# Kernel tuning notes

Measured on AMD Instinct MI355X. Metric: run time of the kernel, lower is better.

The kernel has to match this reference:

```python
import jax, jax.numpy as jnp
import numpy as np

DIM = 2048
N_HEADS = 16
HEAD_DIM = 128
EPS = 1e-6


def setup_inputs() -> dict:
    key = jax.random.key(0)
    ks = jax.random.split(key, 8)
    b, gf, gh, gw = 1, 8, 16, 24
    s = gf * gh * gw
    c = HEAD_DIM // 2
    w = lambda k: 0.02 * jax.random.normal(k, (DIM, DIM), jnp.float32)
    return {
        "x": jax.random.normal(ks[0], (b, s, DIM), jnp.float32),
        "freqs_angle": jax.random.normal(ks[1], (1024, c), jnp.float32),
        "Wq": w(ks[2]), "bq": jnp.zeros((DIM,), jnp.float32),
        "Wk": w(ks[3]), "bk": jnp.zeros((DIM,), jnp.float32),
        "Wv": w(ks[4]), "bv": jnp.zeros((DIM,), jnp.float32),
        "Wo": w(ks[5]), "bo": jnp.zeros((DIM,), jnp.float32),
        "gq": jnp.ones((DIM,), jnp.float32),
        "gk": jnp.ones((DIM,), jnp.float32),
        "seq_len": s, "grid_f": gf, "grid_h": gh, "grid_w": gw,
    }


def _rms(t, g):
    return t * jax.lax.rsqrt(jnp.mean(t * t, axis=-1, keepdims=True) + EPS) * g


def _grid_angles(freqs_angle, gf, gh, gw, c):
    # band split [c - 2*(c//3), c//3, c//3] as in rope_apply
    cf = c - 2 * (c // 3)
    ch = cw = c // 3
    af = freqs_angle[:gf, :cf]            # [F, cf]
    ah = freqs_angle[:gh, cf:cf + ch]     # [H, ch]
    aw = freqs_angle[:gw, cf + ch:c]      # [W, cw]
    ang = jnp.concatenate([
        jnp.broadcast_to(af[:, None, None, :], (gf, gh, gw, cf)),
        jnp.broadcast_to(ah[None, :, None, :], (gf, gh, gw, ch)),
        jnp.broadcast_to(aw[None, None, :, :], (gf, gh, gw, cw)),
    ], axis=-1)
    return ang.reshape(gf * gh * gw, c)   # [s, c]


def reference(x, freqs_angle, Wq, bq, Wk, bk, Wv, bv, Wo, bo, gq, gk,
              seq_len, grid_f, grid_h, grid_w):
    b, s, _ = x.shape
    n, d = N_HEADS, HEAD_DIM
    c = d // 2
    ang = _grid_angles(freqs_angle, grid_f, grid_h, grid_w, c)
    cos = jnp.cos(ang)[None, :, None, :]  # [1, s, 1, c]
    sin = jnp.sin(ang)[None, :, None, :]

    def rope(t):  # complex multiply on (even, odd) = (real, imag) pairs
        te, to = t[..., 0::2], t[..., 1::2]
        return jnp.stack([te * cos - to * sin, te * sin + to * cos], axis=-1).reshape(t.shape)

    q = _rms(x @ Wq.T + bq, gq).reshape(b, s, n, d)
    k = _rms(x @ Wk.T + bk, gk).reshape(b, s, n, d)
    v = (x @ Wv.T + bv).reshape(b, s, n, d)
    q, k = rope(q), rope(k)

    scale = np.float32(1.0 / np.sqrt(d))
    scores = jnp.einsum('bqnd,bknd->bnqk', q, k) * scale
    p = jax.nn.softmax(scores, axis=-1)
    o = jnp.einsum('bnqk,bknd->bqnd', p, v).reshape(b, s, n * d)
    return o @ Wo.T + bo
```

## Files before the change

### kernel.cpp

```cpp
#include <hip/hip_runtime.h>
#include <stdint.h>
#include <stddef.h>

typedef __bf16 bf16_t;
typedef __bf16 bf16x8 __attribute__((ext_vector_type(8)));
typedef __bf16 bf16x4 __attribute__((ext_vector_type(4)));
typedef __bf16 bf16x2 __attribute__((ext_vector_type(2)));
typedef float  f32x4  __attribute__((ext_vector_type(4)));
typedef float  f32x16 __attribute__((ext_vector_type(16)));

#define SEQ   3072
#define DIMD  2048
#define NH    16
#define HD    128
#define QKVN  6144

__device__ __forceinline__ void async16(const bf16_t* g, bf16_t* l) {
  __builtin_amdgcn_global_load_lds((const __attribute__((address_space(1))) uint32_t*)g,
                                   (__attribute__((address_space(3))) uint32_t*)l, 16, 0, 0);
}

__global__ __launch_bounds__(256) void cvt_all(const float* __restrict__ x,
                                               const float* __restrict__ Wq,
                                               const float* __restrict__ Wk,
                                               const float* __restrict__ Wv,
                                               const float* __restrict__ Wo,
                                               const float* __restrict__ bq,
                                               const float* __restrict__ bk,
                                               const float* __restrict__ bv,
                                               bf16_t* __restrict__ xb,
                                               bf16_t* __restrict__ Wqkvb,
                                               bf16_t* __restrict__ Wob,
                                               float* __restrict__ bqkv) {
  const int b = blockIdx.x;
  const float* src; bf16_t* dst; int off;
  if (b < 3072)       { src = x;  dst = xb;              off = b; }
  else if (b < 5120)  { src = Wq; dst = Wqkvb;           off = b - 3072; }
  else if (b < 7168)  { src = Wk; dst = Wqkvb + 4194304; off = b - 5120; }
  else if (b < 9216)  { src = Wv; dst = Wqkvb + 8388608; off = b - 7168; }
  else if (b < 11264) { src = Wo; dst = Wob;             off = b - 9216; }
  else {
    int t = (b - 11264) * 256 + threadIdx.x;
    float v;
    if (t < 2048)      v = bq[t];
    else if (t < 4096) v = bk[t - 2048];
    else               v = bv[t - 4096];
    bqkv[t] = v;
    return;
  }
  const int idx = (off * 256 + threadIdx.x) * 8;
  const float4 a = *(const float4*)(src + idx);
  const float4 c = *(const float4*)(src + idx + 4);
  bf16x8 o;
  o[0] = (bf16_t)a.x; o[1] = (bf16_t)a.y; o[2] = (bf16_t)a.z; o[3] = (bf16_t)a.w;
  o[4] = (bf16_t)c.x; o[5] = (bf16_t)c.y; o[6] = (bf16_t)c.z; o[7] = (bf16_t)c.w;
  *(bf16x8*)(dst + idx) = o;
}

template<bool OUT_BF16>
__global__ __launch_bounds__(256, 3) void gemm_nt(const bf16_t* __restrict__ A,
                                                  const bf16_t* __restrict__ B,
                                                  const float* __restrict__ bias,
                                                  void* __restrict__ Cout,
                                                  int M, int N, int K) {
  __shared__ __align__(16) bf16_t As[128 * 64];
  __shared__ __align__(16) bf16_t Bs[128 * 64];
  const int t = threadIdx.x;
  const int lane = t & 63, wave = t >> 6;
  const int quad = lane >> 4, l15 = lane & 15;
  const int wy = wave >> 1, wx = wave & 1;
  const size_t bm = (size_t)blockIdx.y * 128, bn = (size_t)blockIdx.x * 128;
  const bf16_t* Ab = A + bm * K;
  const bf16_t* Bb = B + bn * K;
  f32x4 acc[4][4] = {};
  int srow[4], scol[4];
#pragma unroll
  for (int r = 0; r < 4; r++) {
    int L = r * 256 + t;
    int row = L >> 3, cp = L & 7;
    srow[r] = row;
    scol[r] = (cp ^ (row & 7)) * 8;
  }
  for (int k0 = 0; k0 < K; k0 += 64) {
    __syncthreads();
#pragma unroll
    for (int r = 0; r < 4; r++)
      async16(Ab + (size_t)srow[r] * K + k0 + scol[r], &As[(r * 256 + t) * 8]);
#pragma unroll
    for (int r = 0; r < 4; r++)
      async16(Bb + (size_t)srow[r] * K + k0 + scol[r], &Bs[(r * 256 + t) * 8]);
    __syncthreads();
#pragma unroll
    for (int ks = 0; ks < 2; ks++) {
      bf16x8 af[4], bfv[4];
#pragma unroll
      for (int i = 0; i < 4; i++) {
        int row = wy * 64 + i * 16 + l15;
        af[i] = *(const bf16x8*)&As[row * 64 + (((ks * 4 + quad) ^ (row & 7)) * 8)];
      }
#pragma unroll
      for (int j = 0; j < 4; j++) {
        int row = wx * 64 + j * 16 + l15;
        bfv[j] = *(const bf16x8*)&Bs[row * 64 + (((ks * 4 + quad) ^ (row & 7)) * 8)];
      }
#pragma unroll
      for (int i = 0; i < 4; i++)
#pragma unroll
        for (int j = 0; j < 4; j++)
          acc[i][j] = __builtin_amdgcn_mfma_f32_16x16x32_bf16(af[i], bfv[j], acc[i][j], 0, 0, 0);
    }
  }
#pragma unroll
  for (int i = 0; i < 4; i++) {
#pragma unroll
    for (int j = 0; j < 4; j++) {
      size_t row = bm + wy * 64 + i * 16 + quad * 4;
      size_t col = bn + wx * 64 + j * 16 + l15;
      float bb = bias[col];
#pragma unroll
      for (int r = 0; r < 4; r++) {
        float v = acc[i][j][r] + bb;
        if (OUT_BF16) ((bf16_t*)Cout)[(row + r) * N + col] = (bf16_t)v;
        else          ((float*)Cout)[(row + r) * N + col] = v;
      }
    }
  }
}

__global__ __launch_bounds__(256) void rmsrope(bf16_t* __restrict__ qkv,
                                               bf16_t* __restrict__ pk,
                                               const float* __restrict__ gq,
                                               const float* __restrict__ gk,
                                               const float* __restrict__ freqs) {
  const int s = blockIdx.x, t = threadIdx.x;
  bf16_t* row = qkv + (size_t)s * QKVN;
  bf16x8 qv = *(const bf16x8*)&row[t * 8];
  bf16x8 kv = *(const bf16x8*)&row[2048 + t * 8];
  float qf[8], kf[8];
  float qs = 0.f, ks2 = 0.f;
#pragma unroll
  for (int i = 0; i < 8; i++) {
    qf[i] = (float)qv[i]; qs  += qf[i] * qf[i];
    kf[i] = (float)kv[i]; ks2 += kf[i] * kf[i];
  }
#pragma unroll
  for (int m = 1; m < 64; m <<= 1) {
    qs  += __shfl_xor(qs, m);
    ks2 += __shfl_xor(ks2, m);
  }
  __shared__ float red[2][4];
  const int wave = t >> 6, lane = t & 63;
  if (lane == 0) { red[0][wave] = qs; red[1][wave] = ks2; }
  __syncthreads();
  qs  = red[0][0] + red[0][1] + red[0][2] + red[0][3];
  ks2 = red[1][0] + red[1][1] + red[1][2] + red[1][3];
  const float qsc = rsqrtf(qs  / 2048.f + 1e-6f) * 0.12751745f;
  const float ksc = rsqrtf(ks2 / 2048.f + 1e-6f);
  const int sf = s / 384, rem = s - sf * 384;
  const int sh = rem / 24, sw = rem - sh * 24;
  bf16x8 qo, ko;
#pragma unroll
  for (int u = 0; u < 4; u++) {
    const int col = t * 8 + 2 * u;
    const int i = (col >> 1) & 63;
    const int frow = (i < 22) ? sf : ((i < 43) ? sh : sw);
    const float ang = freqs[frow * 64 + i];
    float sn, cs;
    __sincosf(ang, &sn, &cs);
    float te = qf[2 * u]     * qsc * gq[col];
    float to = qf[2 * u + 1] * qsc * gq[col + 1];
    qo[2 * u]     = (bf16_t)(te * cs - to * sn);
    qo[2 * u + 1] = (bf16_t)(te * sn + to * cs);
    te = kf[2 * u]     * ksc * gk[col];
    to = kf[2 * u + 1] * ksc * gk[col + 1];
    ko[2 * u]     = (bf16_t)(te * cs - to * sn);
    ko[2 * u + 1] = (bf16_t)(te * sn + to * cs);
  }
  *(bf16x8*)&row[t * 8] = qo;
  *(bf16x8*)&pk[((size_t)(t >> 4) * SEQ + s) * HD + (t & 15) * 8] = ko;
}

__global__ __launch_bounds__(256) void vtrans(const bf16_t* __restrict__ qkv,
                                              bf16_t* __restrict__ pvt) {
  __shared__ bf16_t tile[128][65];
  const int h = blockIdx.y;
  const int s0 = blockIdx.x * 64;
  const int t = threadIdx.x;
#pragma unroll
  for (int r = 0; r < 4; r++) {
    int L = r * 256 + t, s = L >> 4, cp = L & 15;
    bf16x8 v = *(const bf16x8*)&qkv[(size_t)(s0 + s) * QKVN + 4096 + h * HD + cp * 8];
#pragma unroll
    for (int i = 0; i < 8; i++) tile[cp * 8 + i][s] = v[i];
  }
  __syncthreads();
#pragma unroll
  for (int r = 0; r < 4; r++) {
    int L = r * 256 + t, d = L >> 3, c = L & 7;
    bf16x8 o;
#pragma unroll
    for (int i = 0; i < 8; i++) o[i] = tile[d][c * 8 + i];
    *(bf16x8*)&pvt[((size_t)h * HD + d) * SEQ + s0 + c * 8] = o;
  }
}

#define STAGE_KV(BUF, KV1) do {                                              \
    _Pragma("unroll")                                                        \
    for (int r = 0; r < 5; r++) {                                            \
      int L = r * 192 + t;                                                   \
      async16(pkh + (size_t)(KV1) * HD + koff[r], &Ks[BUF][L * 8]);          \
      async16(pvh + (KV1) + voff[r], &Vt[BUF][L * 8]);                       \
    }                                                                        \
    if (t < 64) {                                                            \
      int L = 5 * 192 + t;                                                   \
      async16(pkh + (size_t)(KV1) * HD + koff[5], &Ks[BUF][L * 8]);          \
      async16(pvh + (KV1) + voff[5], &Vt[BUF][L * 8]);                       \
    }                                                                        \
  } while (0)

__global__ __launch_bounds__(192, 2) void flash_attn(const bf16_t* __restrict__ qkv,
                                                     const bf16_t* __restrict__ pk,
                                                     const bf16_t* __restrict__ pvt,
                                                     bf16_t* __restrict__ ob) {
  __shared__ __align__(16) bf16_t Ks[2][64 * 128];
  __shared__ __align__(16) bf16_t Vt[2][128 * 64];
  const int hh = blockIdx.y, qt = blockIdx.x;
  const int s0 = qt * 96;
  const int t = threadIdx.x, wave = t >> 6, lane = t & 63;
  const int l31 = lane & 31, hl = lane >> 5;
  const int wq = wave * 32;
  const bf16_t* pkh = pk  + (size_t)hh * (SEQ * HD);
  const bf16_t* pvh = pvt + (size_t)hh * (HD * SEQ);
  int koff[6], voff[6];
#pragma unroll
  for (int r = 0; r < 6; r++) {
    int L = r * 192 + t;
    int krow = L >> 4, kc = (L & 15) ^ (krow & 7);
    koff[r] = krow * HD + kc * 8;
    int vd = L >> 3, vc = (L & 7) ^ (vd & 7);
    voff[r] = vd * SEQ + vc * 8;
  }
  bf16x8 qfr[8];
#pragma unroll
  for (int ks = 0; ks < 8; ks++)
    qfr[ks] = *(const bf16x8*)&qkv[(size_t)(s0 + wq + l31) * QKVN + hh * HD + ks * 16 + hl * 8];
  bf16x8 vones;
#pragma unroll
  for (int i = 0; i < 8; i++) vones[i] = (bf16_t)1.0f;
  f32x16 oacc[4] = {};
  f32x16 lacc = {};
  STAGE_KV(0, 0);
  for (int kt = 0; kt < SEQ / 64; kt++) {
    const int cur = kt & 1;
    __syncthreads();
    if (kt + 1 < SEQ / 64) STAGE_KV(cur ^ 1, (kt + 1) * 64);
    f32x16 st0 = {}, st1 = {};
    __builtin_amdgcn_s_setprio(1);
#pragma unroll
    for (int ks = 0; ks < 8; ks++) {
      const int r1 = 32 + l31;
      bf16x8 k0 = *(const bf16x8*)&Ks[cur][l31 * 128 + (((ks * 2 + hl) ^ (l31 & 7)) * 8)];
      bf16x8 k1 = *(const bf16x8*)&Ks[cur][r1 * 128 + (((ks * 2 + hl) ^ (r1 & 7)) * 8)];
      st0 = __builtin_amdgcn_mfma_f32_32x32x16_bf16(k0, qfr[ks], st0, 0, 0, 0);
      st1 = __builtin_amdgcn_mfma_f32_32x32x16_bf16(k1, qfr[ks], st1, 0, 0, 0);
    }
    __builtin_amdgcn_s_setprio(0);
    uint32_t c0[8], c1[8];
#pragma unroll
    for (int m = 0; m < 8; m++) {
      bf16x2 w0, w1;
      w0[0] = (bf16_t)__builtin_amdgcn_exp2f(st0[2 * m]);
      w0[1] = (bf16_t)__builtin_amdgcn_exp2f(st0[2 * m + 1]);
      w1[0] = (bf16_t)__builtin_amdgcn_exp2f(st1[2 * m]);
      w1[1] = (bf16_t)__builtin_amdgcn_exp2f(st1[2 * m + 1]);
      c0[m] = __builtin_bit_cast(uint32_t, w0);
      c1[m] = __builtin_bit_cast(uint32_t, w1);
    }
    union U8 { uint32_t u[4]; bf16x8 v; } afr0, afr1, afr2, afr3;
#define BUILD_AFR(DST, CB, B) do {                                           \
      uint32_t sA = hl ? CB[(B) + 0] : CB[(B) + 2];                          \
      uint32_t sB = hl ? CB[(B) + 1] : CB[(B) + 3];                          \
      uint32_t rA = (uint32_t)__shfl_xor((int)sA, 32);                       \
      uint32_t rB = (uint32_t)__shfl_xor((int)sB, 32);                       \
      DST.u[0] = hl ? rA : CB[(B) + 0];                                      \
      DST.u[1] = hl ? rB : CB[(B) + 1];                                      \
      DST.u[2] = hl ? CB[(B) + 2] : rA;                                      \
      DST.u[3] = hl ? CB[(B) + 3] : rB;                                      \
    } while (0)
    BUILD_AFR(afr0, c0, 0);
    BUILD_AFR(afr1, c0, 4);
    BUILD_AFR(afr2, c1, 0);
    BUILD_AFR(afr3, c1, 4);
#undef BUILD_AFR
    __builtin_amdgcn_s_setprio(1);
#define PV_STEP(AFR, S) do {                                                            \
      lacc = __builtin_amdgcn_mfma_f32_32x32x16_bf16(AFR.v, vones, lacc, 0, 0, 0);      \
      _Pragma("unroll")                                                                 \
      for (int dj = 0; dj < 4; dj++) {                                                  \
        const int row = dj * 32 + l31;                                                  \
        bf16x8 vf = *(const bf16x8*)&Vt[cur][row * 64 + ((((S) * 2 + hl) ^ (row & 7)) * 8)]; \
        oacc[dj] = __builtin_amdgcn_mfma_f32_32x32x16_bf16(AFR.v, vf, oacc[dj], 0, 0, 0);    \
      }                                                                                 \
    } while (0)
    PV_STEP(afr0, 0);
    PV_STEP(afr1, 1);
    PV_STEP(afr2, 2);
    PV_STEP(afr3, 3);
#undef PV_STEP
    __builtin_amdgcn_s_setprio(0);
  }
#pragma unroll
  for (int r = 0; r < 16; r++) {
    const float li = 1.f / lacc[r];
    const size_t row = (size_t)(s0 + wq + (r & 3) + 8 * (r >> 2) + 4 * hl);
#pragma unroll
    for (int dj = 0; dj < 4; dj++)
      ob[row * DIMD + hh * HD + dj * 32 + l31] = (bf16_t)(oacc[dj][r] * li);
  }
}

extern "C" void kernel_launch(void* const* d_in, const int* in_sizes, int n_in,
                              void* d_out, int out_size, void* d_ws, size_t ws_size,
                              hipStream_t stream) {
  (void)in_sizes; (void)n_in; (void)out_size;
  const float* x     = (const float*)d_in[0];
  const float* freqs = (const float*)d_in[1];
  const float* Wq    = (const float*)d_in[2];
  const float* bq    = (const float*)d_in[3];
  const float* Wk    = (const float*)d_in[4];
  const float* bk    = (const float*)d_in[5];
  const float* Wv    = (const float*)d_in[6];
  const float* bv    = (const float*)d_in[7];
  const float* Wo    = (const float*)d_in[8];
  const float* bo    = (const float*)d_in[9];
  const float* gq    = (const float*)d_in[10];
  const float* gk    = (const float*)d_in[11];

  char* w = (char*)d_ws;
  bf16_t* xb    = (bf16_t*)(w);
  bf16_t* Wqkvb = (bf16_t*)(w + 12582912);
  bf16_t* Wob   = (bf16_t*)(w + 37748736);
  bf16_t* qkvb  = (bf16_t*)(w + 46137344);
  bf16_t* obuf  = (bf16_t*)(w + 83886080);
  float*  bqkv  = (float*) (w + 96468992);
  bf16_t* pk    = (bf16_t*)(w);
  bf16_t* pvt   = (bf16_t*)(w + 12582912);
  if (ws_size < (size_t)96493568) return;

  cvt_all<<<11288, 256, 0, stream>>>(x, Wq, Wk, Wv, Wo, bq, bk, bv, xb, Wqkvb, Wob, bqkv);

  gemm_nt<true><<<dim3(48, 24), 256, 0, stream>>>(xb, Wqkvb, bqkv, qkvb, SEQ, QKVN, DIMD);
  rmsrope<<<3072, 256, 0, stream>>>(qkvb, pk, gq, gk, freqs);
  vtrans<<<dim3(48, NH), 256, 0, stream>>>(qkvb, pvt);
  flash_attn<<<dim3(32, NH), 192, 0, stream>>>(qkvb, pk, pvt, obuf);
  gemm_nt<false><<<dim3(16, 24), 256, 0, stream>>>(obuf, Wob, bo, (float*)d_out, SEQ, DIMD, DIMD);
}
```

Baseline: 412.7 us.

## Load V fragments directly from global in MFMA-ready layout, drop V LDS staging

The V-transpose kernel now writes V tiles pre-arranged in the exact per-lane MFMA operand order. Flash attention loads these fragments straight from global into registers each iteration instead of staging them through LDS. This halves LDS use and the async copy traffic. The grid is also flattened and remapped so that consecutive workgroups spread across heads, which could improve L2 locality on shared K/V. The costs are 16 more vector registers per lane, which may hurt occupancy, and global-load latency exposed inside the loop without double buffering.

```diff
diff --git a/kernel.cpp b/kernel.cpp
--- a/kernel.cpp
+++ b/kernel.cpp
@@ -181,10 +181,11 @@
 }
 
 __global__ __launch_bounds__(256) void vtrans(const bf16_t* __restrict__ qkv,
-                                              bf16_t* __restrict__ pvt) {
+                                              bf16_t* __restrict__ pvtf) {
   __shared__ bf16_t tile[128][65];
   const int h = blockIdx.y;
-  const int s0 = blockIdx.x * 64;
+  const int kt = blockIdx.x;
+  const int s0 = kt * 64;
   const int t = threadIdx.x;
 #pragma unroll
   for (int r = 0; r < 4; r++) {
@@ -196,49 +197,45 @@
   __syncthreads();
 #pragma unroll
   for (int r = 0; r < 4; r++) {
-    int L = r * 256 + t, d = L >> 3, c = L & 7;
+    int L = r * 256 + t, c = L >> 7, d = L & 127;
     bf16x8 o;
 #pragma unroll
     for (int i = 0; i < 8; i++) o[i] = tile[d][c * 8 + i];
-    *(bf16x8*)&pvt[((size_t)h * HD + d) * SEQ + s0 + c * 8] = o;
-  }
-}
-
-#define STAGE_KV(BUF, KV1) do {                                              \
+    *(bf16x8*)&pvtf[((size_t)h * 48 + kt) * 8192 + (size_t)(((c * 4 + (d >> 5)) * 32 + (d & 31)) * 8)] = o;
+  }
+}
+
+#define STAGE_K(BUF, KV1) do {                                               \
     _Pragma("unroll")                                                        \
     for (int r = 0; r < 5; r++) {                                            \
       int L = r * 192 + t;                                                   \
       async16(pkh + (size_t)(KV1) * HD + koff[r], &Ks[BUF][L * 8]);          \
-      async16(pvh + (KV1) + voff[r], &Vt[BUF][L * 8]);                       \
     }                                                                        \
     if (t < 64) {                                                            \
-      int L = 5 * 192 + t;                                                   \
+      int L = 960 + t;                                                       \
       async16(pkh + (size_t)(KV1) * HD + koff[5], &Ks[BUF][L * 8]);          \
-      async16(pvh + (KV1) + voff[5], &Vt[BUF][L * 8]);                       \
     }                                                                        \
   } while (0)
 
 __global__ __launch_bounds__(192, 2) void flash_attn(const bf16_t* __restrict__ qkv,
                                                      const bf16_t* __restrict__ pk,
-                                                     const bf16_t* __restrict__ pvt,
+                                                     const bf16_t* __restrict__ pvtf,
                                                      bf16_t* __restrict__ ob) {
   __shared__ __align__(16) bf16_t Ks[2][64 * 128];
-  __shared__ __align__(16) bf16_t Vt[2][128 * 64];
-  const int hh = blockIdx.y, qt = blockIdx.x;
+  const int f = blockIdx.x;
+  const int wg = (f & 7) * 64 + (f >> 3);
+  const int hh = wg >> 5, qt = wg & 31;
   const int s0 = qt * 96;
   const int t = threadIdx.x, wave = t >> 6, lane = t & 63;
   const int l31 = lane & 31, hl = lane >> 5;
   const int wq = wave * 32;
-  const bf16_t* pkh = pk  + (size_t)hh * (SEQ * HD);
-  const bf16_t* pvh = pvt + (size_t)hh * (HD * SEQ);
-  int koff[6], voff[6];
+  const bf16_t* pkh = pk + (size_t)hh * (SEQ * HD);
+  int koff[6];
 #pragma unroll
   for (int r = 0; r < 6; r++) {
     int L = r * 192 + t;
     int krow = L >> 4, kc = (L & 15) ^ (krow & 7);
     koff[r] = krow * HD + kc * 8;
-    int vd = L >> 3, vc = (L & 7) ^ (vd & 7);
-    voff[r] = vd * SEQ + vc * 8;
   }
   bf16x8 qfr[8];
 #pragma unroll
@@ -249,11 +246,18 @@
   for (int i = 0; i < 8; i++) vones[i] = (bf16_t)1.0f;
   f32x16 oacc[4] = {};
   f32x16 lacc = {};
-  STAGE_KV(0, 0);
+  STAGE_K(0, 0);
   for (int kt = 0; kt < SEQ / 64; kt++) {
     const int cur = kt & 1;
     __syncthreads();
-    if (kt + 1 < SEQ / 64) STAGE_KV(cur ^ 1, (kt + 1) * 64);
+    if (kt + 1 < SEQ / 64) STAGE_K(cur ^ 1, (kt + 1) * 64);
+    const bf16_t* vfb = pvtf + ((size_t)hh * 48 + kt) * 8192;
+    bf16x8 vf[4][4];
+#pragma unroll
+    for (int S = 0; S < 4; S++)
+#pragma unroll
+      for (int dj = 0; dj < 4; dj++)
+        vf[S][dj] = *(const bf16x8*)&vfb[(size_t)((((S * 2 + hl) * 4 + dj) * 32 + l31) * 8)];
     f32x16 st0 = {}, st1 = {};
     __builtin_amdgcn_s_setprio(1);
 #pragma unroll
@@ -296,11 +300,8 @@
 #define PV_STEP(AFR, S) do {                                                            \
       lacc = __builtin_amdgcn_mfma_f32_32x32x16_bf16(AFR.v, vones, lacc, 0, 0, 0);      \
       _Pragma("unroll")                                                                 \
-      for (int dj = 0; dj < 4; dj++) {                                                  \
-        const int row = dj * 32 + l31;                                                  \
-        bf16x8 vf = *(const bf16x8*)&Vt[cur][row * 64 + ((((S) * 2 + hl) ^ (row & 7)) * 8)]; \
-        oacc[dj] = __builtin_amdgcn_mfma_f32_32x32x16_bf16(AFR.v, vf, oacc[dj], 0, 0, 0);    \
-      }                                                                                 \
+      for (int dj = 0; dj < 4; dj++)                                                    \
+        oacc[dj] = __builtin_amdgcn_mfma_f32_32x32x16_bf16(AFR.v, vf[S][dj], oacc[dj], 0, 0, 0); \
     } while (0)
     PV_STEP(afr0, 0);
     PV_STEP(afr1, 1);
@@ -344,14 +345,14 @@
   bf16_t* obuf  = (bf16_t*)(w + 83886080);
   float*  bqkv  = (float*) (w + 96468992);
   bf16_t* pk    = (bf16_t*)(w);
-  bf16_t* pvt   = (bf16_t*)(w + 12582912);
+  bf16_t* pvtf  = (bf16_t*)(w + 12582912);
   if (ws_size < (size_t)96493568) return;
 
   cvt_all<<<11288, 256, 0, stream>>>(x, Wq, Wk, Wv, Wo, bq, bk, bv, xb, Wqkvb, Wob, bqkv);
 
   gemm_nt<true><<<dim3(48, 24), 256, 0, stream>>>(xb, Wqkvb, bqkv, qkvb, SEQ, QKVN, DIMD);
   rmsrope<<<3072, 256, 0, stream>>>(qkvb, pk, gq, gk, freqs);
-  vtrans<<<dim3(48, NH), 256, 0, stream>>>(qkvb, pvt);
-  flash_attn<<<dim3(32, NH), 192, 0, stream>>>(qkvb, pk, pvt, obuf);
+  vtrans<<<dim3(48, NH), 256, 0, stream>>>(qkvb, pvtf);
+  flash_attn<<<dim3(512), 192, 0, stream>>>(qkvb, pk, pvtf, obuf);
   gemm_nt<false><<<dim3(16, 24), 256, 0, stream>>>(obuf, Wob, bo, (float*)d_out, SEQ, DIMD, DIMD);
 }
```

Result: slower. 485.4 us (+17.6%).
